# Performance work log

Measured on AMD Instinct MI355X. Metric: run time of the kernel, lower is better.

The kernel has to match this reference:

```python
import jax, jax.numpy as jnp
import numpy as np
import math

B, L, D, H = 8, 2048, 1024, 1024


def setup_inputs() -> dict:
    key = jax.random.key(0)
    ks = jax.random.split(key, 6)
    scale = 1.0 / math.sqrt(D)
    return {
        "input_q": jax.random.normal(ks[0], (B, L, D), dtype=jnp.float32),
        "input_k": jax.random.normal(ks[1], (B, L, D), dtype=jnp.float32),
        "k_mask": jax.random.uniform(ks[2], (B, L), dtype=jnp.float32),
        "Wq": jax.random.normal(ks[3], (D, H), dtype=jnp.float32) * scale,
        "bq": jnp.zeros((H,), dtype=jnp.float32),
        "Wk": jax.random.normal(ks[4], (D, H), dtype=jnp.float32) * scale,
        "bk": jnp.zeros((H,), dtype=jnp.float32),
    }


def reference(input_q, input_k, k_mask, Wq, bq, Wk, bk):
    # Linear projections: (b, l, d) @ (d, h) -> (b, l, h)
    q = input_q @ Wq + bq
    k = input_k @ Wk + bk
    # Faithful to original: mask values become 0.0 or -1e9, then an
    # outer product bmm((b,l,1),(b,1,l)) builds the (b,l,l) additive mask.
    m = jnp.where(k_mask > 0.5, 0.0, -1000000000.0)  # (b, l)
    add_mask = m[:, :, None] * m[:, None, :]          # (b, l, l) outer product
    # Scaled dot-product scores
    attn = jnp.einsum("bqh,bkh->bqk", q, k) / math.sqrt(H)
    attn = jax.nn.softmax(attn + add_mask, axis=-1)
    # Weighted sum over the ORIGINAL input_k (not projected k), as in source
    out = jnp.einsum("bqk,bkd->bqd", attn, input_k)
    return out
```

## Files before the change

### kernel.cpp

```cpp
#include <hip/hip_runtime.h>

#define BATCH 8
#define SEQ   2048
#define DIM   1024

typedef __attribute__((ext_vector_type(8)))  short short8;
typedef __attribute__((ext_vector_type(4)))  short short4v;
typedef __attribute__((ext_vector_type(4)))  float floatx4;
typedef __attribute__((ext_vector_type(16))) float floatx16;

__device__ __forceinline__ unsigned short f32_to_bf16(float f) {
    union { float f; unsigned int u; } x; x.f = f;
    unsigned int r = x.u + 0x7fffu + ((x.u >> 16) & 1u);
    return (unsigned short)(r >> 16);
}

__device__ __forceinline__ float bf16_to_f32(unsigned short h) {
    union { unsigned int u; float f; } x; x.u = ((unsigned int)h) << 16;
    return x.f;
}

__device__ __forceinline__ void async_load16(const void* g, void* l) {
    __builtin_amdgcn_global_load_lds(
        (const __attribute__((address_space(1))) void*)g,
        (__attribute__((address_space(3))) void*)l, 16, 0, 0);
}

__global__ __launch_bounds__(256) void prep_misc(
    const float* __restrict__ mask, int* __restrict__ idx,
    int* __restrict__ cnt, int* __restrict__ padcnt, float* __restrict__ mavg,
    const float* __restrict__ Wq, unsigned short* __restrict__ Wqb,
    const float* __restrict__ Wk, unsigned short* __restrict__ Wkb,
    const float* __restrict__ bq, float* __restrict__ g0)
{
    __shared__ int wtot[4];
    __shared__ float rshared[4];
    const int id = blockIdx.x;
    const int t  = threadIdx.x;

    if (id < 8) {
        const int b = id;
        for (int d = t; d < DIM; d += 256) mavg[b * DIM + d] = 0.f;
        const float* mb = mask + b * SEQ;
        int flags[8]; int c = 0;
#pragma unroll
        for (int j = 0; j < 8; ++j) {
            flags[j] = (mb[t * 8 + j] > 0.5f) ? 1 : 0;
            c += flags[j];
        }
        int sc = c;
        for (int o = 1; o < 64; o <<= 1) {
            int v = __shfl_up(sc, o);
            if ((t & 63) >= o) sc += v;
        }
        const int lane = t & 63, wave = t >> 6;
        if (lane == 63) wtot[wave] = sc;
        __syncthreads();
        int woff = 0;
        for (int w = 0; w < wave; ++w) woff += wtot[w];
        int p = woff + sc - c;
#pragma unroll
        for (int j = 0; j < 8; ++j)
            if (flags[j]) idx[b * SEQ + (p++)] = t * 8 + j;
        __syncthreads();
        const int total = wtot[0] + wtot[1] + wtot[2] + wtot[3];
        if (t == 0) { cnt[b] = total; padcnt[b] = (total + 127) & ~127; }
        for (int q = total + t; q < SEQ; q += 256) idx[b * SEQ + q] = 0;
    } else if (id < 1032) {
        const int k = id - 8;
        const float* src = (k < 512) ? Wq : Wk;
        unsigned short* dst = (k < 512) ? Wqb : Wkb;
        const long i = ((long)(k & 511) * 256 + t) * 8;
        floatx4 v0 = *(const floatx4*)(src + i);
        floatx4 v1 = *(const floatx4*)(src + i + 4);
        short8 w;
#pragma unroll
        for (int j = 0; j < 4; ++j) w[j]     = (short)f32_to_bf16(v0[j]);
#pragma unroll
        for (int j = 0; j < 4; ++j) w[4 + j] = (short)f32_to_bf16(v1[j]);
        *(short8*)(dst + i) = w;
    } else {
        const int n = id - 1032;
        float s = 0.f;
        for (int h = t; h < DIM; h += 256) s += bq[h] * Wk[(long)n * DIM + h];
        for (int o = 32; o; o >>= 1) s += __shfl_xor(s, o);
        if ((t & 63) == 0) rshared[t >> 6] = s;
        __syncthreads();
        if (t == 0) g0[n] = rshared[0] + rshared[1] + rshared[2] + rshared[3];
    }
}

template<bool C_BF16, bool BIAS, bool LIMIT, bool SCATTER>
__device__ __forceinline__ void gemm_tile_128(
    unsigned short* __restrict__ As, unsigned short* __restrict__ Bs,
    int bx, int by, int bz,
    const unsigned short* __restrict__ A, const unsigned short* __restrict__ Bt,
    void* __restrict__ Cp, const float* __restrict__ bias,
    int N, int K, long sA, long sB, long sC, float scale,
    const int* __restrict__ mlim, const int* __restrict__ cntp,
    const int* __restrict__ idx)
{
    const int row0 = bx * 128;
    if (LIMIT && row0 >= mlim[bz]) return;

    const int tid  = threadIdx.x;
    const int lane = tid & 63;
    const int wave = tid >> 6;
    const int wm   = wave >> 1;
    const int wn   = wave & 1;
    const int l31  = lane & 31;
    const int half = lane >> 5;
    const int x7   = lane & 7;
    const int col0 = by * 128;

    const int sr = lane >> 3;
    const int sq = ((lane & 7) ^ sr) * 8;

    const long K8 = (long)K * 8;
    const unsigned short* aRow =
        A + (long)bz * sA + (long)row0 * K + (long)(wave * 32 + sr) * K + sq;
    const unsigned short* bRow =
        Bt + (long)bz * sB + (long)col0 * K + (long)(wave * 32 + sr) * K + sq;

    floatx16 acc[2][2];
#pragma unroll
    for (int a = 0; a < 2; ++a)
#pragma unroll
        for (int b = 0; b < 2; ++b)
#pragma unroll
            for (int r = 0; r < 16; ++r) acc[a][b][r] = 0.f;

    const int raf[2] = { (wm * 64 +  0 + l31) * 64, (wm * 64 + 32 + l31) * 64 };
    const int rbf[2] = { (wn * 64 +  0 + l31) * 64, (wn * 64 + 32 + l31) * 64 };

    for (int kt = 0; kt < K; kt += 64) {
#pragma unroll
        for (int c = 0; c < 4; ++c) {
            const int chunk = wave * 4 + c;
            async_load16(aRow + kt + c * K8, As + chunk * 512);
            async_load16(bRow + kt + c * K8, Bs + chunk * 512);
        }
        __syncthreads();

#pragma unroll
        for (int ks = 0; ks < 4; ++ks) {
            const int sw = ((ks * 2 + half) ^ x7) << 3;
            short8 af[2], bf[2];
#pragma unroll
            for (int t = 0; t < 2; ++t) {
                af[t] = *(const short8*)(As + raf[t] + sw);
                bf[t] = *(const short8*)(Bs + rbf[t] + sw);
            }
#pragma unroll
            for (int tm = 0; tm < 2; ++tm)
#pragma unroll
                for (int tn = 0; tn < 2; ++tn)
                    acc[tm][tn] = __builtin_amdgcn_mfma_f32_32x32x16_bf16(
                        af[tm], bf[tn], acc[tm][tn], 0, 0, 0);
        }
        __syncthreads();
    }

    const long zC = (long)bz * sC;
    const int climit = SCATTER ? cntp[bz] : 0;
    const int* ridx  = SCATTER ? (idx + bz * SEQ) : (const int*)nullptr;
#pragma unroll
    for (int tn = 0; tn < 2; ++tn) {
        const int ccol = col0 + wn * 64 + tn * 32 + l31;
        float bv = 0.f;
        if (BIAS) bv = bias[ccol];
#pragma unroll
        for (int tm = 0; tm < 2; ++tm) {
            const int rbase = row0 + wm * 64 + tm * 32 + 4 * half;
#pragma unroll
            for (int r = 0; r < 16; ++r) {
                const int crow = rbase + (r & 3) + 8 * (r >> 2);
                float v = acc[tm][tn][r] * scale + bv;
                long orow = crow;
                if (SCATTER) {
                    if (crow >= climit) continue;
                    orow = ridx[crow];
                }
                const long ci = zC + orow * (long)N + ccol;
                if (C_BF16) ((unsigned short*)Cp)[ci] = f32_to_bf16(v);
                else        ((float*)Cp)[ci] = v;
            }
        }
    }
}

template<bool C_BF16, bool BIAS, bool LIMIT, bool SCATTER, int FLAT, bool MFILL>
__global__ __launch_bounds__(256, 4) void gemm_bt(
    const unsigned short* __restrict__ A, const unsigned short* __restrict__ Bt,
    void* __restrict__ Cp, const float* __restrict__ bias,
    int N, int K, long sA, long sB, long sC, float scale,
    const int* __restrict__ mlim, const int* __restrict__ cntp,
    const int* __restrict__ idx, int sh,
    const float* __restrict__ kmask, const float* __restrict__ fmavg)
{
    __shared__ unsigned short As[128 * 64];
    __shared__ unsigned short Bs[128 * 64];

    if (MFILL && blockIdx.x >= 1024) {
        const int id2 = blockIdx.x - 1024;
        const int b = id2 >> 8;
        const int row = ((id2 & 255) << 3) + (threadIdx.x >> 5);
        if (kmask[b * SEQ + row] <= 0.5f) {
            const float inv = 1.0f / (float)(SEQ - cntp[b]);
            float* ob = (float*)Cp + ((long)b * SEQ + row) * DIM;
            const float* mv = fmavg + b * DIM;
            const int l32 = threadIdx.x & 31;
#pragma unroll
            for (int i = 0; i < 8; ++i) {
                const int d = (l32 + i * 32) * 4;
                const floatx4 s = *(const floatx4*)(mv + d);
                floatx4 o;
#pragma unroll
                for (int j = 0; j < 4; ++j) o[j] = s[j] * inv;
                *(floatx4*)(ob + d) = o;
            }
        }
        return;
    }

    int bx, by, bz;
    if (FLAT == 0) {
        bx = blockIdx.x; by = blockIdx.y; bz = blockIdx.z;
    } else {
        const int id = blockIdx.x;
        bz = id & 7;
        const int rem = id >> 3;
        const int m = (1 << sh) - 1;
        if (FLAT == 1) { bx = rem & m; by = rem >> sh; }
        else           { by = rem & m; bx = rem >> sh; }
    }
    gemm_tile_128<C_BF16, BIAS, LIMIT, SCATTER>(
        As, Bs, bx, by, bz, A, Bt, Cp, bias, N, K, sA, sB, sC, scale,
        mlim, cntp, idx);
}

__global__ __launch_bounds__(256, 4) void fused_stage2(
    const unsigned short* __restrict__ Wkb, const unsigned short* __restrict__ Wqb,
    unsigned short* __restrict__ Gt,
    const float* __restrict__ xq, const int* __restrict__ idx,
    const int* __restrict__ padcnt, unsigned short* __restrict__ qc,
    const float* __restrict__ xk, const float* __restrict__ mask,
    unsigned short* __restrict__ kbf, unsigned short* __restrict__ Vt,
    float* __restrict__ mavg)
{
    __shared__ unsigned short sbuf[2 * 128 * 64];
    const int id = blockIdx.x;

    if (id < 64) {
        gemm_tile_128<true, false, false, false>(
            sbuf, sbuf + 128 * 64, id & 7, id >> 3, 0,
            Wkb, Wqb, Gt, nullptr, DIM, DIM, 0, 0, 0, 1.0f,
            nullptr, nullptr, nullptr);
    } else if (id < 64 + 4096) {
        const int p  = id - 64;
        const int c0 = (p & 15) * 64;
        const int r0 = ((p >> 4) & 31) * 64;
        const int b  = p >> 9;
        float* tile = (float*)sbuf;
        float* msk  = tile + 64 * 65;
        float* csum = msk + 64;
        const int cg = threadIdx.x & 15;
        const int rr = threadIdx.x >> 4;
        const float* xb = xk + (long)b * SEQ * DIM;
        unsigned short* kb = kbf + (long)b * SEQ * DIM;
        unsigned short* vb = Vt + (long)b * DIM * SEQ;

        if (threadIdx.x < 64) msk[threadIdx.x] = mask[b * SEQ + r0 + threadIdx.x];

#pragma unroll
        for (int i = 0; i < 4; ++i) {
            const int row = rr + i * 16;
            const floatx4 v = *(const floatx4*)(xb + (long)(r0 + row) * DIM + c0 + cg * 4);
            short4v w;
#pragma unroll
            for (int j = 0; j < 4; ++j) {
                tile[row * 65 + cg * 4 + j] = v[j];
                w[j] = (short)f32_to_bf16(v[j]);
            }
            *(short4v*)(kb + (long)(r0 + row) * DIM + c0 + cg * 4) = w;
        }
        __syncthreads();

        {
            const int rgroup = threadIdx.x >> 6;
            const int c = threadIdx.x & 63;
            float s = 0.f;
#pragma unroll
            for (int r = 0; r < 16; ++r) {
                const int row = rgroup * 16 + r;
                s += (msk[row] <= 0.5f) ? tile[row * 65 + c] : 0.f;
            }
            csum[rgroup * 64 + c] = s;
        }

        {
            const int sg = threadIdx.x & 15;
            const int ch = threadIdx.x >> 4;
#pragma unroll
            for (int i = 0; i < 4; ++i) {
                const int c = ch + i * 16;
                short4v w;
#pragma unroll
                for (int j = 0; j < 4; ++j)
                    w[j] = (short)f32_to_bf16(tile[(sg * 4 + j) * 65 + c]);
                *(short4v*)(vb + (long)(c0 + c) * SEQ + r0 + sg * 4) = w;
            }
        }
        __syncthreads();
        if (threadIdx.x < 64) {
            const int c = threadIdx.x;
            const float tot = csum[0 * 64 + c] + csum[1 * 64 + c] +
                              csum[2 * 64 + c] + csum[3 * 64 + c];
            atomicAdd(&mavg[b * DIM + c0 + c], tot);
        }
    } else {
        const int g  = id - (64 + 4096);
        const int b  = g >> 8;
        const int rc = ((g & 255) << 3) + (threadIdx.x >> 5);
        if (rc < padcnt[b]) {
            const int src = idx[b * SEQ + rc];
            const int l32 = threadIdx.x & 31;
            const float* s = xq + ((long)b * SEQ + src) * DIM;
            unsigned short* d = qc + ((long)b * SEQ + rc) * DIM;
#pragma unroll
            for (int i = 0; i < 8; ++i) {
                const int c = (l32 + i * 32) * 4;
                const floatx4 v = *(const floatx4*)(s + c);
                short4v w;
#pragma unroll
                for (int j = 0; j < 4; ++j) w[j] = (short)f32_to_bf16(v[j]);
                *(short4v*)(d + c) = w;
            }
        }
    }
}

__global__ __launch_bounds__(256) void softmax_rows(
    unsigned short* __restrict__ S, const int* __restrict__ padcnt)
{
    const int b = blockIdx.x >> 11, rc = blockIdx.x & 2047;
    if (rc >= padcnt[b]) return;
    const long base = (long)blockIdx.x * SEQ + threadIdx.x * 8;
    const int lane = threadIdx.x & 63, wave = threadIdx.x >> 6;
    __shared__ float rbuf[8];

    short8 v = *(const short8*)(S + base);
    float x[8];
#pragma unroll
    for (int j = 0; j < 8; ++j) x[j] = bf16_to_f32((unsigned short)v[j]);

    float m = x[0];
#pragma unroll
    for (int j = 1; j < 8; ++j) m = fmaxf(m, x[j]);
    for (int o = 32; o; o >>= 1) m = fmaxf(m, __shfl_xor(m, o));
    if (lane == 0) rbuf[wave] = m;
    __syncthreads();
    m = fmaxf(fmaxf(rbuf[0], rbuf[1]), fmaxf(rbuf[2], rbuf[3]));

    float e[8], s = 0.f;
#pragma unroll
    for (int j = 0; j < 8; ++j) { e[j] = __expf(x[j] - m); s += e[j]; }
    for (int o = 32; o; o >>= 1) s += __shfl_xor(s, o);
    if (lane == 0) rbuf[4 + wave] = s;
    __syncthreads();
    s = rbuf[4] + rbuf[5] + rbuf[6] + rbuf[7];
    const float inv = 1.0f / s;

    short8 o8;
#pragma unroll
    for (int j = 0; j < 8; ++j) o8[j] = (short)f32_to_bf16(e[j] * inv);
    *(short8*)(S + base) = o8;
}

extern "C" void kernel_launch(void* const* d_in, const int* in_sizes, int n_in,
                              void* d_out, int out_size, void* d_ws, size_t ws_size,
                              hipStream_t stream) {
    (void)in_sizes; (void)n_in; (void)out_size;
    const float* input_q = (const float*)d_in[0];
    const float* input_k = (const float*)d_in[1];
    const float* k_mask  = (const float*)d_in[2];
    const float* Wq      = (const float*)d_in[3];
    const float* bq      = (const float*)d_in[4];
    const float* Wk      = (const float*)d_in[5];
    const float* bk      = (const float*)d_in[6];
    (void)bk;
    float* out = (float*)d_out;

    char* ws = (char*)d_ws;
    unsigned short* qc   = (unsigned short*)(ws);
    unsigned short* S    = (unsigned short*)(ws);
    unsigned short* qpp  = (unsigned short*)(ws + 67108864);
    unsigned short* Wqb  = (unsigned short*)(ws + 67108864);
    unsigned short* Wkb  = (unsigned short*)(ws + 69206016);
    unsigned short* kbf  = (unsigned short*)(ws + 100663296);
    unsigned short* Vt   = (unsigned short*)(ws + 134217728);
    unsigned short* Gt   = (unsigned short*)(ws + 167772160);
    float*          g0   = (float*)(ws + 169869312);
    float*          mavg = (float*)(ws + 169873408);
    int*            idx  = (int*)(ws + 169906176);
    int*            cnts = (int*)(ws + 169971712);
    int*            pcnt = (int*)(ws + 169971744);
    if (ws_size < 169971776) return;

    prep_misc<<<2056, 256, 0, stream>>>(k_mask, idx, cnts, pcnt, mavg,
                                        Wq, Wqb, Wk, Wkb, bq, g0);

    fused_stage2<<<64 + 4096 + 2048, 256, 0, stream>>>(
        Wkb, Wqb, Gt, input_q, idx, pcnt, qc, input_k, k_mask, kbf, Vt, mavg);

    gemm_bt<true, true, true, false, 2, false><<<8 * 16 * 8, 256, 0, stream>>>(
        qc, Gt, qpp, g0, DIM, DIM,
        (long)SEQ * DIM, 0, (long)SEQ * DIM, 1.0f,
        pcnt, nullptr, nullptr, 3, nullptr, nullptr);

    gemm_bt<true, false, true, false, 1, false><<<8 * 16 * 16, 256, 0, stream>>>(
        qpp, kbf, S, nullptr, SEQ, DIM,
        (long)SEQ * DIM, (long)SEQ * DIM, (long)SEQ * SEQ, 0.03125f,
        pcnt, nullptr, nullptr, 4, nullptr, nullptr);

    softmax_rows<<<BATCH * SEQ, 256, 0, stream>>>(S, pcnt);

    gemm_bt<false, false, true, true, 2, true><<<1024 + 2048, 256, 0, stream>>>(
        S, Vt, out, nullptr, DIM, SEQ,
        (long)SEQ * SEQ, (long)DIM * SEQ, (long)SEQ * DIM, 1.0f,
        pcnt, cnts, idx, 3, k_mask, mavg);
}
```

Baseline: 324.7 us.

## Fuse softmax into score GEMM epilogue and PV GEMM normalization

Removes the separate softmax kernel. The score GEMM epilogue now applies exp directly and accumulates per-row sums through atomics into a rowsum buffer, which extra blocks of the projection GEMM zero beforehand. The PV GEMM then scales its output rows by the inverse row sum. This saves a full read and write pass over the score matrix, at the cost of atomics and of dropping the max subtraction, so large scores could overflow exp.

```diff
diff --git a/kernel.cpp b/kernel.cpp
--- a/kernel.cpp
+++ b/kernel.cpp
@@ -90,7 +90,7 @@
     }
 }
 
-template<bool C_BF16, bool BIAS, bool LIMIT, bool SCATTER>
+template<bool C_BF16, bool BIAS, bool LIMIT, bool SCATTER, bool EXPSUM, bool NORM>
 __device__ __forceinline__ void gemm_tile_128(
     unsigned short* __restrict__ As, unsigned short* __restrict__ Bs,
     int bx, int by, int bz,
@@ -98,7 +98,7 @@
     void* __restrict__ Cp, const float* __restrict__ bias,
     int N, int K, long sA, long sB, long sC, float scale,
     const int* __restrict__ mlim, const int* __restrict__ cntp,
-    const int* __restrict__ idx)
+    const int* __restrict__ idx, float* __restrict__ rowsum)
 {
     const int row0 = bx * 128;
     if (LIMIT && row0 >= mlim[bz]) return;
@@ -165,17 +165,33 @@
     const int climit = SCATTER ? cntp[bz] : 0;
     const int* ridx  = SCATTER ? (idx + bz * SEQ) : (const int*)nullptr;
 #pragma unroll
-    for (int tn = 0; tn < 2; ++tn) {
-        const int ccol = col0 + wn * 64 + tn * 32 + l31;
-        float bv = 0.f;
-        if (BIAS) bv = bias[ccol];
-#pragma unroll
-        for (int tm = 0; tm < 2; ++tm) {
-            const int rbase = row0 + wm * 64 + tm * 32 + 4 * half;
+    for (int tm = 0; tm < 2; ++tm) {
+        const int rbase = row0 + wm * 64 + tm * 32 + 4 * half;
+        float esum[16];
+        float rsinv[16];
+        if (EXPSUM) {
+#pragma unroll
+            for (int r = 0; r < 16; ++r) esum[r] = 0.f;
+        }
+        if (NORM) {
+#pragma unroll
+            for (int r = 0; r < 16; ++r) {
+                const int crow = rbase + (r & 3) + 8 * (r >> 2);
+                rsinv[r] = (!SCATTER || crow < climit)
+                               ? 1.0f / rowsum[(long)bz * SEQ + crow] : 0.f;
+            }
+        }
+#pragma unroll
+        for (int tn = 0; tn < 2; ++tn) {
+            const int ccol = col0 + wn * 64 + tn * 32 + l31;
+            float bv = 0.f;
+            if (BIAS) bv = bias[ccol];
 #pragma unroll
             for (int r = 0; r < 16; ++r) {
                 const int crow = rbase + (r & 3) + 8 * (r >> 2);
                 float v = acc[tm][tn][r] * scale + bv;
+                if (EXPSUM) { v = __expf(v); esum[r] += v; }
+                if (NORM)   { v = acc[tm][tn][r] * rsinv[r]; }
                 long orow = crow;
                 if (SCATTER) {
                     if (crow >= climit) continue;
@@ -186,22 +202,37 @@
                 else        ((float*)Cp)[ci] = v;
             }
         }
-    }
-}
-
-template<bool C_BF16, bool BIAS, bool LIMIT, bool SCATTER, int FLAT, bool MFILL>
+        if (EXPSUM) {
+#pragma unroll
+            for (int r = 0; r < 16; ++r) {
+                float s = esum[r];
+                s += __shfl_xor(s, 1);  s += __shfl_xor(s, 2);
+                s += __shfl_xor(s, 4);  s += __shfl_xor(s, 8);
+                s += __shfl_xor(s, 16);
+                if (l31 == 0) {
+                    const int crow = rbase + (r & 3) + 8 * (r >> 2);
+                    atomicAdd(&rowsum[(long)bz * SEQ + crow], s);
+                }
+            }
+        }
+    }
+}
+
+template<bool C_BF16, bool BIAS, bool LIMIT, bool SCATTER, int FLAT, int XROLE,
+         bool EXPSUM, bool NORM>
 __global__ __launch_bounds__(256, 4) void gemm_bt(
     const unsigned short* __restrict__ A, const unsigned short* __restrict__ Bt,
     void* __restrict__ Cp, const float* __restrict__ bias,
     int N, int K, long sA, long sB, long sC, float scale,
     const int* __restrict__ mlim, const int* __restrict__ cntp,
     const int* __restrict__ idx, int sh,
-    const float* __restrict__ kmask, const float* __restrict__ fmavg)
+    const float* __restrict__ kmask, const float* __restrict__ fmavg,
+    float* __restrict__ rowsum)
 {
     __shared__ unsigned short As[128 * 64];
     __shared__ unsigned short Bs[128 * 64];
 
-    if (MFILL && blockIdx.x >= 1024) {
+    if (XROLE == 1 && blockIdx.x >= 1024) {
         const int id2 = blockIdx.x - 1024;
         const int b = id2 >> 8;
         const int row = ((id2 & 255) << 3) + (threadIdx.x >> 5);
@@ -220,6 +251,12 @@
                 *(floatx4*)(ob + d) = o;
             }
         }
+        return;
+    }
+    if (XROLE == 2 && blockIdx.x >= 1024) {
+        const int b = blockIdx.x - 1024;
+        float* rs = rowsum + b * SEQ;
+        for (int i = threadIdx.x; i < SEQ; i += 256) rs[i] = 0.f;
         return;
     }
 
@@ -234,9 +271,9 @@
         if (FLAT == 1) { bx = rem & m; by = rem >> sh; }
         else           { by = rem & m; bx = rem >> sh; }
     }
-    gemm_tile_128<C_BF16, BIAS, LIMIT, SCATTER>(
+    gemm_tile_128<C_BF16, BIAS, LIMIT, SCATTER, EXPSUM, NORM>(
         As, Bs, bx, by, bz, A, Bt, Cp, bias, N, K, sA, sB, sC, scale,
-        mlim, cntp, idx);
+        mlim, cntp, idx, rowsum);
 }
 
 __global__ __launch_bounds__(256, 4) void fused_stage2(
@@ -252,10 +289,10 @@
     const int id = blockIdx.x;
 
     if (id < 64) {
-        gemm_tile_128<true, false, false, false>(
+        gemm_tile_128<true, false, false, false, false, false>(
             sbuf, sbuf + 128 * 64, id & 7, id >> 3, 0,
             Wkb, Wqb, Gt, nullptr, DIM, DIM, 0, 0, 0, 1.0f,
-            nullptr, nullptr, nullptr);
+            nullptr, nullptr, nullptr, nullptr);
     } else if (id < 64 + 4096) {
         const int p  = id - 64;
         const int c0 = (p & 15) * 64;
@@ -340,43 +377,6 @@
     }
 }
 
-__global__ __launch_bounds__(256) void softmax_rows(
-    unsigned short* __restrict__ S, const int* __restrict__ padcnt)
-{
-    const int b = blockIdx.x >> 11, rc = blockIdx.x & 2047;
-    if (rc >= padcnt[b]) return;
-    const long base = (long)blockIdx.x * SEQ + threadIdx.x * 8;
-    const int lane = threadIdx.x & 63, wave = threadIdx.x >> 6;
-    __shared__ float rbuf[8];
-
-    short8 v = *(const short8*)(S + base);
-    float x[8];
-#pragma unroll
-    for (int j = 0; j < 8; ++j) x[j] = bf16_to_f32((unsigned short)v[j]);
-
-    float m = x[0];
-#pragma unroll
-    for (int j = 1; j < 8; ++j) m = fmaxf(m, x[j]);
-    for (int o = 32; o; o >>= 1) m = fmaxf(m, __shfl_xor(m, o));
-    if (lane == 0) rbuf[wave] = m;
-    __syncthreads();
-    m = fmaxf(fmaxf(rbuf[0], rbuf[1]), fmaxf(rbuf[2], rbuf[3]));
-
-    float e[8], s = 0.f;
-#pragma unroll
-    for (int j = 0; j < 8; ++j) { e[j] = __expf(x[j] - m); s += e[j]; }
-    for (int o = 32; o; o >>= 1) s += __shfl_xor(s, o);
-    if (lane == 0) rbuf[4 + wave] = s;
-    __syncthreads();
-    s = rbuf[4] + rbuf[5] + rbuf[6] + rbuf[7];
-    const float inv = 1.0f / s;
-
-    short8 o8;
-#pragma unroll
-    for (int j = 0; j < 8; ++j) o8[j] = (short)f32_to_bf16(e[j] * inv);
-    *(short8*)(S + base) = o8;
-}
-
 extern "C" void kernel_launch(void* const* d_in, const int* in_sizes, int n_in,
                               void* d_out, int out_size, void* d_ws, size_t ws_size,
                               hipStream_t stream) {
@@ -397,6 +397,7 @@
     unsigned short* qpp  = (unsigned short*)(ws + 67108864);
     unsigned short* Wqb  = (unsigned short*)(ws + 67108864);
     unsigned short* Wkb  = (unsigned short*)(ws + 69206016);
+    float*          rowsum = (float*)(ws + 70254592);
     unsigned short* kbf  = (unsigned short*)(ws + 100663296);
     unsigned short* Vt   = (unsigned short*)(ws + 134217728);
     unsigned short* Gt   = (unsigned short*)(ws + 167772160);
@@ -413,20 +414,18 @@
     fused_stage2<<<64 + 4096 + 2048, 256, 0, stream>>>(
         Wkb, Wqb, Gt, input_q, idx, pcnt, qc, input_k, k_mask, kbf, Vt, mavg);
 
-    gemm_bt<true, true, true, false, 2, false><<<8 * 16 * 8, 256, 0, stream>>>(
+    gemm_bt<true, true, true, false, 2, 2, false, false><<<1024 + 8, 256, 0, stream>>>(
         qc, Gt, qpp, g0, DIM, DIM,
         (long)SEQ * DIM, 0, (long)SEQ * DIM, 1.0f,
-        pcnt, nullptr, nullptr, 3, nullptr, nullptr);
-
-    gemm_bt<true, false, true, false, 1, false><<<8 * 16 * 16, 256, 0, stream>>>(
+        pcnt, nullptr, nullptr, 3, nullptr, nullptr, rowsum);
+
+    gemm_bt<true, false, true, false, 1, 0, true, false><<<8 * 16 * 16, 256, 0, stream>>>(
         qpp, kbf, S, nullptr, SEQ, DIM,
         (long)SEQ * DIM, (long)SEQ * DIM, (long)SEQ * SEQ, 0.03125f,
-        pcnt, nullptr, nullptr, 4, nullptr, nullptr);
-
-    softmax_rows<<<BATCH * SEQ, 256, 0, stream>>>(S, pcnt);
-
-    gemm_bt<false, false, true, true, 2, true><<<1024 + 2048, 256, 0, stream>>>(
+        pcnt, nullptr, nullptr, 4, nullptr, nullptr, rowsum);
+
+    gemm_bt<false, false, true, true, 2, 1, false, true><<<1024 + 2048, 256, 0, stream>>>(
         S, Vt, out, nullptr, DIM, SEQ,
         (long)SEQ * SEQ, (long)DIM * SEQ, (long)SEQ * DIM, 1.0f,
-        pcnt, cnts, idx, 3, k_mask, mavg);
-}
+        pcnt, cnts, idx, 3, k_mask, mavg, rowsum);
+}
```

After: 327.7 us. No clear change (+0.9%).
